# Kernel optimization log

Measured on AMD Instinct MI355X. Metric: run time of the kernel, lower is better.

## Reference

```python
import jax, jax.numpy as jnp
import numpy as np

N = 50000
E = 1600000
D_IN = 128
D_OUT = 128
BN_EPS = 1e-5


def setup_inputs() -> dict:
    key = jax.random.key(0)
    ks = jax.random.split(key, 8)
    x = jax.random.normal(ks[0], (N, D_IN), dtype=jnp.float32)
    local_edge_index = jax.random.randint(ks[1], (2, E), 0, N, dtype=jnp.int64)
    global_edge_index = jax.random.randint(ks[2], (2, E), 0, N, dtype=jnp.int64)
    # torch nn.Linear weights are [out_features, in_features]
    scale = 1.0 / np.sqrt(D_IN)
    W1 = jax.random.uniform(ks[3], (D_OUT, D_IN), jnp.float32, -scale, scale)
    W2_local = jax.random.uniform(ks[4], (D_OUT, D_IN), jnp.float32, -scale, scale)
    W2_global = jax.random.uniform(ks[5], (D_OUT, D_IN), jnp.float32, -scale, scale)
    gamma = jnp.ones((D_OUT,), jnp.float32)
    beta = jnp.zeros((D_OUT,), jnp.float32)
    return {"x": x, "local_edge_index": local_edge_index,
            "global_edge_index": global_edge_index,
            "W1": W1, "W2_local": W2_local, "W2_global": W2_global,
            "gamma": gamma, "beta": beta}


def _aggregate(x, edge_index, W):
    # gather neighbor feats, transform, scatter-add to rows
    row, col = edge_index[0], edge_index[1]
    neigh = x[col] @ W.T                       # [E, D_OUT]
    return jax.ops.segment_sum(neigh, row, num_segments=x.shape[0])


def reference(x, local_edge_index, global_edge_index, W1, W2_local, W2_global, gamma, beta):
    out = x @ W1.T                              # [N, D_OUT]
    out = out + _aggregate(x, local_edge_index, W2_local)
    out = out + _aggregate(x, global_edge_index, W2_global)
    # BatchNorm1d in training mode: biased batch statistics over nodes
    mean = jnp.mean(out, axis=0)
    var = jnp.mean(jnp.square(out - mean), axis=0)
    out = (out - mean) * jax.lax.rsqrt(var + BN_EPS) * gamma + beta
    return jax.nn.relu(out)
```

## Files before the change

kernel.cpp:

```cpp
#include <hip/hip_runtime.h>

#define D 128
#define BN_EPS 1e-5f

__global__ __launch_bounds__(256) void convert_kernel(
    const float* __restrict__ x, ushort* __restrict__ xbf, int total8) {
  int t = blockIdx.x * 256 + threadIdx.x;
  if (t >= total8) return;
  const float4* p = reinterpret_cast<const float4*>(x) + (size_t)t * 2;
  float4 a = p[0], b = p[1];
  float v[8] = {a.x, a.y, a.z, a.w, b.x, b.y, b.z, b.w};
  uint r[8];
#pragma unroll
  for (int j = 0; j < 8; ++j) {
    uint bits = __float_as_uint(v[j]);
    r[j] = (bits + 0x7FFFu + ((bits >> 16) & 1u)) >> 16;
  }
  uint4 o;
  o.x = r[0] | (r[1] << 16); o.y = r[2] | (r[3] << 16);
  o.z = r[4] | (r[5] << 16); o.w = r[6] | (r[7] << 16);
  *reinterpret_cast<uint4*>(xbf + (size_t)t * 8) = o;
}

__global__ __launch_bounds__(256) void hist_kernel(
    const int* __restrict__ ei, int* __restrict__ deg, int E) {
  int t = blockIdx.x * blockDim.x + threadIdx.x;
  if (t < E) atomicAdd(&deg[ei[t]], 1);
}

__global__ __launch_bounds__(1024) void scan_kernel(
    const int* __restrict__ deg, int* __restrict__ off, int n) {
  __shared__ int ls[1024];
  const int t = threadIdx.x;
  const int chunk = (n + 1023) / 1024;
  const int lo = t * chunk;
  const int hi = (lo + chunk < n) ? lo + chunk : n;
  int s = 0;
  for (int j = lo; j < hi; ++j) s += deg[j];
  ls[t] = s;
  __syncthreads();
  for (int d = 1; d < 1024; d <<= 1) {
    int v = (t >= d) ? ls[t - d] : 0;
    __syncthreads();
    ls[t] += v;
    __syncthreads();
  }
  int run = (t == 0) ? 0 : ls[t - 1];
  for (int j = lo; j < hi; ++j) { off[j] = run; run += deg[j]; }
}

__global__ __launch_bounds__(256) void fill_kernel(
    const int* __restrict__ ei, int* __restrict__ off,
    int* __restrict__ csr, int E) {
  int t = blockIdx.x * blockDim.x + threadIdx.x;
  if (t < E) {
    int dst = ei[t];
    int src = ei[E + t];
    int p = atomicAdd(&off[dst], 1);
    csr[p] = src;
  }
}

__global__ __launch_bounds__(256) void gather_kernel(
    const ushort* __restrict__ xbf, const int* __restrict__ csr,
    const int* __restrict__ off_end, const int* __restrict__ deg,
    float* __restrict__ agg, int n) {
  const int wid = (blockIdx.x * 256 + threadIdx.x) >> 6;
  const int lane = threadIdx.x & 63;
  if (wid >= n) return;
  const int end = off_end[wid];
  const int beg = end - deg[wid];
  float ax = 0.f, ay = 0.f;
  int e = beg;
  while (e < end) {
    int m = end - e; if (m > 64) m = 64;
    int pick = lane < m ? lane : m - 1;
    int myidx = csr[e + pick];
    int j = 0;
    for (; j + 4 <= m; j += 4) {
      int s0 = __shfl(myidx, j + 0);
      int s1 = __shfl(myidx, j + 1);
      int s2 = __shfl(myidx, j + 2);
      int s3 = __shfl(myidx, j + 3);
      uint v0 = reinterpret_cast<const uint*>(xbf + (size_t)s0 * D)[lane];
      uint v1 = reinterpret_cast<const uint*>(xbf + (size_t)s1 * D)[lane];
      uint v2 = reinterpret_cast<const uint*>(xbf + (size_t)s2 * D)[lane];
      uint v3 = reinterpret_cast<const uint*>(xbf + (size_t)s3 * D)[lane];
      ax += __uint_as_float(v0 << 16) + __uint_as_float(v1 << 16)
          + __uint_as_float(v2 << 16) + __uint_as_float(v3 << 16);
      ay += __uint_as_float(v0 & 0xFFFF0000u) + __uint_as_float(v1 & 0xFFFF0000u)
          + __uint_as_float(v2 & 0xFFFF0000u) + __uint_as_float(v3 & 0xFFFF0000u);
    }
    for (; j < m; ++j) {
      int s = __shfl(myidx, j);
      uint v = reinterpret_cast<const uint*>(xbf + (size_t)s * D)[lane];
      ax += __uint_as_float(v << 16);
      ay += __uint_as_float(v & 0xFFFF0000u);
    }
    e += m;
  }
  *reinterpret_cast<float2*>(agg + (size_t)wid * D + lane * 2) = make_float2(ax, ay);
}

__global__ __launch_bounds__(256) void gemm3_kernel(
    const float* __restrict__ x, const float* __restrict__ aggL,
    const float* __restrict__ aggG, const float* __restrict__ W1,
    const float* __restrict__ W2l, const float* __restrict__ W2g,
    float* __restrict__ pre, int n) {
  __shared__ float xs[64][36];
  __shared__ float wsh[128][36];
  const int tid = threadIdx.x;
  const int ty = tid >> 4;
  const int tx = tid & 15;
  const int nodeBase = blockIdx.x * 64;

  float acc[4][8];
#pragma unroll
  for (int i = 0; i < 4; ++i)
#pragma unroll
    for (int j = 0; j < 8; ++j) acc[i][j] = 0.f;

  const float* ins[3] = {x, aggL, aggG};
  const float* wts[3] = {W1, W2l, W2g};

  for (int p = 0; p < 3; ++p) {
    const float* __restrict__ A = ins[p];
    const float* __restrict__ Wp = wts[p];
    for (int kc = 0; kc < D; kc += 32) {
      __syncthreads();
#pragma unroll
      for (int i = 0; i < 2; ++i) {
        int lin = tid + i * 256;
        int r = lin >> 3, q = lin & 7;
        int node = nodeBase + r;
        float4 v = make_float4(0.f, 0.f, 0.f, 0.f);
        if (node < n)
          v = *reinterpret_cast<const float4*>(A + (size_t)node * D + kc + q * 4);
        *reinterpret_cast<float4*>(&xs[r][q * 4]) = v;
      }
#pragma unroll
      for (int i = 0; i < 4; ++i) {
        int lin = tid + i * 256;
        int r = lin >> 3, q = lin & 7;
        *reinterpret_cast<float4*>(&wsh[r][q * 4]) =
            *reinterpret_cast<const float4*>(Wp + (size_t)r * D + kc + q * 4);
      }
      __syncthreads();
#pragma unroll
      for (int k = 0; k < 32; k += 4) {
        float4 a4[4], b4[8];
#pragma unroll
        for (int i = 0; i < 4; ++i) a4[i] = *reinterpret_cast<const float4*>(&xs[ty + 16 * i][k]);
#pragma unroll
        for (int j = 0; j < 8; ++j) b4[j] = *reinterpret_cast<const float4*>(&wsh[tx + 16 * j][k]);
#pragma unroll
        for (int i = 0; i < 4; ++i)
#pragma unroll
          for (int j = 0; j < 8; ++j)
            acc[i][j] += a4[i].x * b4[j].x + a4[i].y * b4[j].y +
                         a4[i].z * b4[j].z + a4[i].w * b4[j].w;
      }
    }
  }

#pragma unroll
  for (int i = 0; i < 4; ++i) {
    int node = nodeBase + ty + 16 * i;
    if (node < n) {
#pragma unroll
      for (int j = 0; j < 8; ++j)
        pre[(size_t)node * D + tx + 16 * j] = acc[i][j];
    }
  }
}

__global__ __launch_bounds__(256) void stats_kernel(
    const float* __restrict__ pre, float* __restrict__ sums,
    float* __restrict__ sumsq, int n) {
  const int f = threadIdx.x & 127;
  const int g = threadIdx.x >> 7;
  const int base = blockIdx.x * 256;
  float s = 0.f, s2 = 0.f;
  int lim = base + 256 < n ? base + 256 : n;
  for (int r = base + g; r < lim; r += 2) {
    float v = pre[(size_t)r * D + f];
    s += v;
    s2 += v * v;
  }
  __shared__ float bufs[128], bufs2[128];
  if (g) { bufs[f] = s; bufs2[f] = s2; }
  __syncthreads();
  if (!g) {
    unsafeAtomicAdd(&sums[f], s + bufs[f]);
    unsafeAtomicAdd(&sumsq[f], s2 + bufs2[f]);
  }
}

__global__ void bnparam_kernel(const float* __restrict__ sums,
                               const float* __restrict__ sumsq,
                               const float* __restrict__ gamma,
                               const float* __restrict__ beta,
                               float* __restrict__ scale,
                               float* __restrict__ shift, int n) {
  int f = threadIdx.x;
  float inv_n = 1.f / (float)n;
  float mean = sums[f] * inv_n;
  float var = sumsq[f] * inv_n - mean * mean;
  float sc = rsqrtf(var + BN_EPS) * gamma[f];
  scale[f] = sc;
  shift[f] = beta[f] - mean * sc;
}

__global__ __launch_bounds__(256) void norm_relu_kernel(
    float* __restrict__ buf, const float* __restrict__ scale,
    const float* __restrict__ shift, size_t total4) {
  size_t idx = (size_t)blockIdx.x * blockDim.x + threadIdx.x;
  if (idx >= total4) return;
  size_t i = idx * 4;
  float4 v = *reinterpret_cast<const float4*>(buf + i);
  int f = (int)(i & 127);
  v.x = fmaxf(v.x * scale[f + 0] + shift[f + 0], 0.f);
  v.y = fmaxf(v.y * scale[f + 1] + shift[f + 1], 0.f);
  v.z = fmaxf(v.z * scale[f + 2] + shift[f + 2], 0.f);
  v.w = fmaxf(v.w * scale[f + 3] + shift[f + 3], 0.f);
  *reinterpret_cast<float4*>(buf + i) = v;
}

extern "C" void kernel_launch(void* const* d_in, const int* in_sizes, int n_in,
                              void* d_out, int out_size, void* d_ws, size_t ws_size,
                              hipStream_t stream) {
  const float* x     = (const float*)d_in[0];
  const int*   eiL   = (const int*)d_in[1];
  const int*   eiG   = (const int*)d_in[2];
  const float* W1    = (const float*)d_in[3];
  const float* W2l   = (const float*)d_in[4];
  const float* W2g   = (const float*)d_in[5];
  const float* gamma = (const float*)d_in[6];
  const float* beta  = (const float*)d_in[7];

  const int n = in_sizes[0] / D;
  const int E = in_sizes[1] / 2;
  const size_t nd = (size_t)n * D;

  float* ws    = (float*)d_ws;
  float* aggL  = ws;
  float* aggG  = ws + nd;
  float* sums  = ws + 2 * nd;
  float* sumsq = sums + 128;
  float* scale = sums + 256;
  float* shift = sums + 384;
  int*   deg   = (int*)(sums + 512);
  int*   off   = deg + n;
  int*   csr   = off + n;
  ushort* xbf  = (ushort*)(csr + E);
  float* pre   = (float*)d_out;

  const int eblk = (E + 255) / 256;
  const int gblk = ((n * 64) + 255) / 256;

  convert_kernel<<<((int)(nd / 8) + 255) / 256, 256, 0, stream>>>(x, xbf, (int)(nd / 8));
  hipMemsetAsync(sums, 0, 256 * sizeof(float), stream);

  hipMemsetAsync(deg, 0, n * sizeof(int), stream);
  hist_kernel<<<eblk, 256, 0, stream>>>(eiL, deg, E);
  scan_kernel<<<1, 1024, 0, stream>>>(deg, off, n);
  fill_kernel<<<eblk, 256, 0, stream>>>(eiL, off, csr, E);
  gather_kernel<<<gblk, 256, 0, stream>>>(xbf, csr, off, deg, aggL, n);

  hipMemsetAsync(deg, 0, n * sizeof(int), stream);
  hist_kernel<<<eblk, 256, 0, stream>>>(eiG, deg, E);
  scan_kernel<<<1, 1024, 0, stream>>>(deg, off, n);
  fill_kernel<<<eblk, 256, 0, stream>>>(eiG, off, csr, E);
  gather_kernel<<<gblk, 256, 0, stream>>>(xbf, csr, off, deg, aggG, n);

  gemm3_kernel<<<(n + 63) / 64, 256, 0, stream>>>(x, aggL, aggG, W1, W2l, W2g, pre, n);

  stats_kernel<<<(n + 255) / 256, 256, 0, stream>>>(pre, sums, sumsq, n);
  bnparam_kernel<<<1, 128, 0, stream>>>(sums, sumsq, gamma, beta, scale, shift, n);
  {
    size_t total4 = nd / 4;
    int nblk = (int)((total4 + 255) / 256);
    norm_relu_kernel<<<nblk, 256, 0, stream>>>(pre, scale, shift, total4);
  }
}
```

Baseline: 986.1 us.

## Replace FP32 SIMT GEMM with bf16 MFMA and store aggregates as bf16

The gather kernels now round their fp32 neighbour sums to bf16 and write half as many bytes. The weights are converted to bf16 once per call. A new GEMM kernel uses bf16 16x16x32 MFMA instructions on 128-row tiles instead of the fp32 FMA-based tiled GEMM. This is meant to cut GEMM compute time and the traffic for storing and reloading the aggregates. The cost is lower precision in the inputs and aggregates, which could affect accuracy tolerance.

```diff
diff --git a/kernel.cpp b/kernel.cpp
--- a/kernel.cpp
+++ b/kernel.cpp
@@ -2,6 +2,9 @@
 
 #define D 128
 #define BN_EPS 1e-5f
+
+typedef float f32x4 __attribute__((ext_vector_type(4)));
+typedef short bf16x8 __attribute__((ext_vector_type(8)));
 
 __global__ __launch_bounds__(256) void convert_kernel(
     const float* __restrict__ x, ushort* __restrict__ xbf, int total8) {
@@ -64,7 +67,7 @@
 __global__ __launch_bounds__(256) void gather_kernel(
     const ushort* __restrict__ xbf, const int* __restrict__ csr,
     const int* __restrict__ off_end, const int* __restrict__ deg,
-    float* __restrict__ agg, int n) {
+    ushort* __restrict__ agg, int n) {
   const int wid = (blockIdx.x * 256 + threadIdx.x) >> 6;
   const int lane = threadIdx.x & 63;
   if (wid >= n) return;
@@ -99,77 +102,75 @@
     }
     e += m;
   }
-  *reinterpret_cast<float2*>(agg + (size_t)wid * D + lane * 2) = make_float2(ax, ay);
-}
-
-__global__ __launch_bounds__(256) void gemm3_kernel(
-    const float* __restrict__ x, const float* __restrict__ aggL,
-    const float* __restrict__ aggG, const float* __restrict__ W1,
-    const float* __restrict__ W2l, const float* __restrict__ W2g,
+  uint bx = __float_as_uint(ax);
+  uint by = __float_as_uint(ay);
+  uint rx = (bx + 0x7FFFu + ((bx >> 16) & 1u)) >> 16;
+  uint ry = (by + 0x7FFFu + ((by >> 16) & 1u)) >> 16;
+  reinterpret_cast<uint*>(agg)[(size_t)wid * 64 + lane] = rx | (ry << 16);
+}
+
+__global__ __launch_bounds__(256) void gemm3_mfma(
+    const ushort* __restrict__ xbf, const ushort* __restrict__ aggLb,
+    const ushort* __restrict__ aggGb, const ushort* __restrict__ Wb,
     float* __restrict__ pre, int n) {
-  __shared__ float xs[64][36];
-  __shared__ float wsh[128][36];
+  __shared__ ushort As[128][40];
+  __shared__ ushort Bs[128][40];
   const int tid = threadIdx.x;
-  const int ty = tid >> 4;
-  const int tx = tid & 15;
-  const int nodeBase = blockIdx.x * 64;
-
-  float acc[4][8];
+  const int wave = tid >> 6, lane = tid & 63;
+  const int wm = wave >> 1, wn = wave & 1;
+  const int rowBase = blockIdx.x * 128;
+  const int l15 = lane & 15, lhi8 = (lane >> 4) * 8;
+
+  f32x4 acc[4][4];
 #pragma unroll
   for (int i = 0; i < 4; ++i)
 #pragma unroll
-    for (int j = 0; j < 8; ++j) acc[i][j] = 0.f;
-
-  const float* ins[3] = {x, aggL, aggG};
-  const float* wts[3] = {W1, W2l, W2g};
+    for (int j = 0; j < 4; ++j) acc[i][j] = (f32x4)(0.f);
 
   for (int p = 0; p < 3; ++p) {
-    const float* __restrict__ A = ins[p];
-    const float* __restrict__ Wp = wts[p];
+    const ushort* __restrict__ A = (p == 0) ? xbf : (p == 1 ? aggLb : aggGb);
+    const ushort* __restrict__ W = Wb + p * 16384;
     for (int kc = 0; kc < D; kc += 32) {
       __syncthreads();
 #pragma unroll
       for (int i = 0; i < 2; ++i) {
-        int lin = tid + i * 256;
-        int r = lin >> 3, q = lin & 7;
-        int node = nodeBase + r;
-        float4 v = make_float4(0.f, 0.f, 0.f, 0.f);
+        int c = tid + i * 256;
+        int r = c >> 2, q = (c & 3) * 8;
+        int node = rowBase + r;
+        uint4 va = make_uint4(0, 0, 0, 0);
         if (node < n)
-          v = *reinterpret_cast<const float4*>(A + (size_t)node * D + kc + q * 4);
-        *reinterpret_cast<float4*>(&xs[r][q * 4]) = v;
-      }
-#pragma unroll
-      for (int i = 0; i < 4; ++i) {
-        int lin = tid + i * 256;
-        int r = lin >> 3, q = lin & 7;
-        *reinterpret_cast<float4*>(&wsh[r][q * 4]) =
-            *reinterpret_cast<const float4*>(Wp + (size_t)r * D + kc + q * 4);
+          va = *reinterpret_cast<const uint4*>(A + (size_t)node * D + kc + q);
+        *reinterpret_cast<uint4*>(&As[r][q]) = va;
+        *reinterpret_cast<uint4*>(&Bs[r][q]) =
+            *reinterpret_cast<const uint4*>(W + (size_t)r * D + kc + q);
       }
       __syncthreads();
-#pragma unroll
-      for (int k = 0; k < 32; k += 4) {
-        float4 a4[4], b4[8];
-#pragma unroll
-        for (int i = 0; i < 4; ++i) a4[i] = *reinterpret_cast<const float4*>(&xs[ty + 16 * i][k]);
-#pragma unroll
-        for (int j = 0; j < 8; ++j) b4[j] = *reinterpret_cast<const float4*>(&wsh[tx + 16 * j][k]);
-#pragma unroll
-        for (int i = 0; i < 4; ++i)
-#pragma unroll
-          for (int j = 0; j < 8; ++j)
-            acc[i][j] += a4[i].x * b4[j].x + a4[i].y * b4[j].y +
-                         a4[i].z * b4[j].z + a4[i].w * b4[j].w;
+      bf16x8 af[4], bf[4];
+#pragma unroll
+      for (int mi = 0; mi < 4; ++mi)
+        af[mi] = *reinterpret_cast<const bf16x8*>(&As[wm * 64 + mi * 16 + l15][lhi8]);
+#pragma unroll
+      for (int ni = 0; ni < 4; ++ni)
+        bf[ni] = *reinterpret_cast<const bf16x8*>(&Bs[wn * 64 + ni * 16 + l15][lhi8]);
+#pragma unroll
+      for (int mi = 0; mi < 4; ++mi)
+#pragma unroll
+        for (int ni = 0; ni < 4; ++ni)
+          acc[mi][ni] = __builtin_amdgcn_mfma_f32_16x16x32_bf16(
+              af[mi], bf[ni], acc[mi][ni], 0, 0, 0);
+    }
+  }
+
+#pragma unroll
+  for (int mi = 0; mi < 4; ++mi) {
+#pragma unroll
+    for (int j = 0; j < 4; ++j) {
+      int row = rowBase + wm * 64 + mi * 16 + (lane >> 4) * 4 + j;
+      if (row < n) {
+        float* o = pre + (size_t)row * D + wn * 64 + l15;
+#pragma unroll
+        for (int ni = 0; ni < 4; ++ni) o[ni * 16] = acc[mi][ni][j];
       }
-    }
-  }
-
-#pragma unroll
-  for (int i = 0; i < 4; ++i) {
-    int node = nodeBase + ty + 16 * i;
-    if (node < n) {
-#pragma unroll
-      for (int j = 0; j < 8; ++j)
-        pre[(size_t)node * D + tx + 16 * j] = acc[i][j];
     }
   }
 }
@@ -243,37 +244,41 @@
   const size_t nd = (size_t)n * D;
 
   float* ws    = (float*)d_ws;
-  float* aggL  = ws;
-  float* aggG  = ws + nd;
-  float* sums  = ws + 2 * nd;
+  float* sums  = ws;
   float* sumsq = sums + 128;
   float* scale = sums + 256;
   float* shift = sums + 384;
   int*   deg   = (int*)(sums + 512);
   int*   off   = deg + n;
   int*   csr   = off + n;
-  ushort* xbf  = (ushort*)(csr + E);
+  ushort* xbf   = (ushort*)(csr + E);
+  ushort* aggLb = xbf + nd;
+  ushort* aggGb = aggLb + nd;
+  ushort* Wb    = aggGb + nd;
   float* pre   = (float*)d_out;
 
   const int eblk = (E + 255) / 256;
   const int gblk = ((n * 64) + 255) / 256;
 
   convert_kernel<<<((int)(nd / 8) + 255) / 256, 256, 0, stream>>>(x, xbf, (int)(nd / 8));
+  convert_kernel<<<8, 256, 0, stream>>>(W1,  Wb,          2048);
+  convert_kernel<<<8, 256, 0, stream>>>(W2l, Wb + 16384,  2048);
+  convert_kernel<<<8, 256, 0, stream>>>(W2g, Wb + 32768,  2048);
   hipMemsetAsync(sums, 0, 256 * sizeof(float), stream);
 
   hipMemsetAsync(deg, 0, n * sizeof(int), stream);
   hist_kernel<<<eblk, 256, 0, stream>>>(eiL, deg, E);
   scan_kernel<<<1, 1024, 0, stream>>>(deg, off, n);
   fill_kernel<<<eblk, 256, 0, stream>>>(eiL, off, csr, E);
-  gather_kernel<<<gblk, 256, 0, stream>>>(xbf, csr, off, deg, aggL, n);
+  gather_kernel<<<gblk, 256, 0, stream>>>(xbf, csr, off, deg, aggLb, n);
 
   hipMemsetAsync(deg, 0, n * sizeof(int), stream);
   hist_kernel<<<eblk, 256, 0, stream>>>(eiG, deg, E);
   scan_kernel<<<1, 1024, 0, stream>>>(deg, off, n);
   fill_kernel<<<eblk, 256, 0, stream>>>(eiG, off, csr, E);
-  gather_kernel<<<gblk, 256, 0, stream>>>(xbf, csr, off, deg, aggG, n);
-
-  gemm3_kernel<<<(n + 63) / 64, 256, 0, stream>>>(x, aggL, aggG, W1, W2l, W2g, pre, n);
+  gather_kernel<<<gblk, 256, 0, stream>>>(xbf, csr, off, deg, aggGb, n);
+
+  gemm3_mfma<<<(n + 127) / 128, 256, 0, stream>>>(xbf, aggLb, aggGb, Wb, pre, n);
 
   stats_kernel<<<(n + 255) / 256, 256, 0, stream>>>(pre, sums, sumsq, n);
   bnparam_kernel<<<1, 128, 0, stream>>>(sums, sumsq, gamma, beta, scale, shift, n);
```

Result: faster. 793.3 us (-19.5%).
